# Kernel optimization log

Hardware: AMD Instinct MI355X
Metric: run time of the kernel (lower is better)

## Reference

```python
import math
import jax, jax.numpy as jnp
import numpy as np

NGRAM = 2
NUM_HEADS = 16
EMBED_DIM = 1024
HEAD_DIM = EMBED_DIM // NUM_HEADS
NUM_BUCKETS = 32
MAX_DIST = 128
REAL_T = 512
BSZ = 4
NEG = -10000.0


def _bucket_np(n):
    # unidirectional T5-style log bucket, matching _relative_positions_bucket
    n = np.maximum(n, 0)
    max_exact = NUM_BUCKETS // 2
    is_small = n < max_exact
    val = max_exact + np.log(np.maximum(n, 1) / max_exact) / math.log(MAX_DIST / max_exact) * (NUM_BUCKETS - max_exact)
    val = np.minimum(val, NUM_BUCKETS - 1).astype(np.int32)
    return np.where(is_small, n.astype(np.int32), val)


def setup_inputs() -> dict:
    key = jax.random.key(0)
    ks = jax.random.split(key, 4)
    T, B, E = REAL_T, BSZ, EMBED_DIM
    hidden_states = jax.random.normal(ks[0], ((1 + NGRAM) * T, B, E), jnp.float32)
    s = 1.0 / math.sqrt(E)  # ~xavier scale
    in_proj_weight = jax.random.uniform(ks[1], (3 * E, E), jnp.float32, -s, s)
    in_proj_bias = jnp.zeros((3 * E,), jnp.float32)
    rel_w = jax.random.uniform(ks[2], (NUM_BUCKETS * NUM_HEADS, E), jnp.float32, -s, s)
    rel_b = jnp.zeros((NUM_BUCKETS * NUM_HEADS,), jnp.float32)
    out_w = jax.random.uniform(ks[3], (E, E), jnp.float32, -s, s)
    out_b = jnp.zeros((E,), jnp.float32)
    # relative-position buckets (main stream: keys at positions 1..T)
    pos = np.arange(1, T + 1)
    i_buckets_main = np.broadcast_to(_bucket_np(pos[:, None] - pos[None, :]), (B, T, T)).copy()
    # predict stream keys: concat(main positions shifted by -1, predict positions)
    key_pos = np.concatenate([pos - 1, pos])
    i_buckets_ngram = np.broadcast_to(_bucket_np(pos[:, None] - key_pos[None, :]), (B, T, 2 * T)).copy()
    # masks
    t = np.arange(T)
    self_attn_mask = np.where(t[None, :] <= t[:, None], 0.0, NEG).astype(np.float32)  # causal [T,T]
    s_idx = np.arange(2 * T)
    allow = ((s_idx[None, :] < T) & (s_idx[None, :] <= t[:, None])) | (s_idx[None, :] == T + t[:, None])
    ngram_mask = np.broadcast_to(np.where(allow, 0.0, NEG).astype(np.float32), (NGRAM, T, 2 * T)).copy()
    return dict(
        hidden_states=hidden_states,
        in_proj_weight=in_proj_weight, in_proj_bias=in_proj_bias,
        rel_w=rel_w, rel_b=rel_b, out_w=out_w, out_b=out_b,
        self_attn_mask=jnp.asarray(self_attn_mask), ngram_mask=jnp.asarray(ngram_mask),
        i_buckets_main=jnp.asarray(i_buckets_main, jnp.int32),
        i_buckets_ngram=jnp.asarray(i_buckets_ngram, jnp.int32),
    )


def _rel_values(h, rel_w, rel_b):
    # h: [..., T, E] -> per-head bucket values [..., H, T, NUM_BUCKETS]
    vals = h @ rel_w.T + rel_b                              # [..., T, K*H]
    vals = vals.reshape(vals.shape[:-1] + (NUM_BUCKETS, NUM_HEADS))  # [..., T, K, H]
    return jnp.moveaxis(vals, (-1, -2), (-3, -1))           # [..., H, T, K]


def _forward(hidden_states, in_proj_weight, in_proj_bias, rel_w, rel_b, out_w, out_b,
             self_attn_mask, ngram_mask, i_buckets_main, i_buckets_ngram):
    tgt_len, B, E = hidden_states.shape
    T = tgt_len // (1 + NGRAM)
    H, d = NUM_HEADS, HEAD_DIM
    scaling = d ** -0.5

    qkv = hidden_states @ in_proj_weight.T + in_proj_bias
    q, k, v = jnp.split(qkv, 3, axis=-1)
    q = q * scaling

    def to_bh(x):  # [tgt_len, B, E] -> [B*H, tgt_len, d]
        return jnp.swapaxes(x.reshape(tgt_len, B * H, d), 0, 1)

    q, k, v = to_bh(q), to_bh(k), to_bh(v)
    q_main, k_main, v_main = q[:, :T], k[:, :T], v[:, :T]

    # ---- main stream ----
    aw_main = jnp.einsum('btd,bsd->bts', q_main, k_main)            # [BH,T,T]
    h_main = jnp.swapaxes(hidden_states[:T], 0, 1)                  # [B,T,E]
    vals_main = _rel_values(h_main, rel_w, rel_b)                   # [B,H,T,K]
    idx = jnp.broadcast_to(i_buckets_main[:, None], (B, H, T, T))
    rel_main = jnp.take_along_axis(vals_main, idx, axis=-1).reshape(B * H, T, T)
    aw_main = aw_main + rel_main + self_attn_mask[None]
    p_main = jax.nn.softmax(aw_main.astype(jnp.float32), axis=-1).astype(aw_main.dtype)
    attn_main = jnp.einsum('bts,bsd->btd', p_main, v_main)          # [BH,T,d]
    attn_main = jnp.swapaxes(attn_main, 0, 1).reshape(T, B, E) @ out_w.T + out_b

    # ---- ngram (predict) streams ----
    S2 = 2 * T
    q_ng = jnp.moveaxis(q[:, T:].reshape(B * H, NGRAM, T, d), 1, 0)  # [N,BH,T,d]
    k_ng = jnp.moveaxis(k[:, T:].reshape(B * H, NGRAM, T, d), 1, 0)
    v_ng = jnp.moveaxis(v[:, T:].reshape(B * H, NGRAM, T, d), 1, 0)
    k_cat = jnp.concatenate([jnp.broadcast_to(k_main[None], (NGRAM, B * H, T, d)), k_ng], axis=2)  # [N,BH,2T,d]
    v_cat = jnp.concatenate([jnp.broadcast_to(v_main[None], (NGRAM, B * H, T, d)), v_ng], axis=2)
    aw_ng = jnp.einsum('nbtd,nbsd->nbts', q_ng, k_cat)               # [N,BH,T,2T]
    h_ng = jnp.swapaxes(hidden_states[T:].reshape(NGRAM, T, B, E), 1, 2)  # [N,B,T,E]
    vals_ng = _rel_values(h_ng, rel_w, rel_b)                        # [N,B,H,T,K]
    idx2 = jnp.broadcast_to(i_buckets_ngram[None, :, None], (NGRAM, B, H, T, S2))
    rel_ng = jnp.take_along_axis(vals_ng, idx2, axis=-1).reshape(NGRAM, B * H, T, S2)
    aw_ng = aw_ng + rel_ng + ngram_mask[:, None]
    p_ng = jax.nn.softmax(aw_ng.astype(jnp.float32), axis=-1).astype(aw_ng.dtype)
    attn_ng = jnp.einsum('nbts,nbsd->nbtd', p_ng, v_cat)             # [N,BH,T,d]
    attn_ng = jnp.swapaxes(attn_ng, 1, 2).reshape(NGRAM, T, B, E) @ out_w.T + out_b

    return jnp.concatenate([attn_main, attn_ng.reshape(NGRAM * T, B, E)], axis=0)  # [(1+N)T,B,E]


def reference(hidden_states, in_proj_weight, in_proj_bias, rel_w, rel_b, out_w, out_b,
              self_attn_mask, ngram_mask, i_buckets_main, i_buckets_ngram):
    return _forward(hidden_states, in_proj_weight, in_proj_bias, rel_w, rel_b, out_w, out_b,
                    self_attn_mask, ngram_mask, i_buckets_main, i_buckets_ngram)
```

## Files before the change

kernel.cpp:

```cpp
#include <hip/hip_runtime.h>
#include <stdint.h>

#define T_LEN 512
#define NTOK  1536
#define EMB   1024
#define BS    4

typedef __bf16 bf16x8 __attribute__((ext_vector_type(8)));
typedef float  f32x4  __attribute__((ext_vector_type(4)));

__device__ __forceinline__ float bflo(unsigned short u){
  union { unsigned int i; float f; } a; a.i = ((unsigned int)u) << 16; return a.f;
}
__device__ __forceinline__ unsigned short f2bf(float f){
  union { float f; unsigned int i; } v; v.f = f;
  unsigned int x = v.i;
  return (unsigned short)((x + 0x7fffu + ((x >> 16) & 1u)) >> 16);
}

__device__ __forceinline__ void gld_lds16(const unsigned short* gptr, unsigned short* lptr){
  __builtin_amdgcn_global_load_lds(
      (const __attribute__((address_space(1))) unsigned int*)gptr,
      (__attribute__((address_space(3))) unsigned int*)lptr, 16, 0, 0);
}

__global__ __launch_bounds__(256)
void cast_k(const float* __restrict__ h, const float* __restrict__ wq,
            const float* __restrict__ rw, const float* __restrict__ ow,
            unsigned short* __restrict__ Hb, unsigned short* __restrict__ Wc,
            unsigned short* __restrict__ Ob)
{
  const size_t e = ((size_t)blockIdx.x * 256 + threadIdx.x) * 8;
  const float* src; unsigned short* dst;
  if (e < 6291456)            { src = h  + e;                 dst = Hb + e; }
  else if (e < 9437184)       { size_t o = e - 6291456;       src = wq + o; dst = Wc + o; }
  else if (e < 9961472)       { size_t o = e - 9437184;       src = rw + o; dst = Wc + 3145728 + o; }
  else                        { size_t o = e - 9961472;       src = ow + o; dst = Ob + o; }
  float4 f0 = *(const float4*)src, f1 = *(const float4*)(src + 4);
  unsigned short r[8];
  r[0]=f2bf(f0.x); r[1]=f2bf(f0.y); r[2]=f2bf(f0.z); r[3]=f2bf(f0.w);
  r[4]=f2bf(f1.x); r[5]=f2bf(f1.y); r[6]=f2bf(f1.z); r[7]=f2bf(f1.w);
  *(uint4*)dst = *(const uint4*)r;
}

template<int MODE>
__global__ __launch_bounds__(256)
void mgemm(const unsigned short* __restrict__ A,
           const unsigned short* __restrict__ W,
           const float* __restrict__ B0,
           const float* __restrict__ B1,
           unsigned short* __restrict__ Qo, unsigned short* __restrict__ Ko,
           unsigned short* __restrict__ Vo, float* __restrict__ VALS,
           float* __restrict__ OUT)
{
  constexpr int TM = (MODE == 0) ? 128 : 64;
  constexpr int NI = (MODE == 0) ? 4 : 2;
  __shared__ unsigned short As[TM*32];
  __shared__ unsigned short Bs[128*32];
  const int K = 1024;
  const int m0 = blockIdx.y * TM, n0 = blockIdx.x * 128;
  const int tid = threadIdx.x;
  const int wid = tid >> 6, lane = tid & 63;
  const int l15 = lane & 15, q8 = (lane >> 4) * 8;
  const int srow = lane >> 2, schunk = (lane & 3) * 8;
  const int wcol = (MODE == 0) ? (wid >> 1) * 64 : wid * 32;
  const int wtok = (MODE == 0) ? (wid & 1) * 64 : 0;

  f32x4 acc[NI][4];
  #pragma unroll
  for (int i=0;i<NI;i++)
    #pragma unroll
    for (int j=0;j<4;j++)
      #pragma unroll
      for (int r=0;r<4;r++) acc[i][j][r] = 0.f;

  for (int k0 = 0; k0 < K; k0 += 32) {
    if (MODE == 0) {
      #pragma unroll
      for (int p = 0; p < 2; ++p) {
        const int r0 = p*64 + wid*16;
        gld_lds16(A + (size_t)(m0 + r0 + srow)*K + k0 + schunk, &As[r0*32]);
      }
    } else {
      const int r0 = wid*16;
      gld_lds16(A + (size_t)(m0 + r0 + srow)*K + k0 + schunk, &As[r0*32]);
    }
    #pragma unroll
    for (int p = 0; p < 2; ++p) {
      const int r0 = p*64 + wid*16;
      gld_lds16(W + (size_t)(n0 + r0 + srow)*K + k0 + schunk, &Bs[r0*32]);
    }
    __syncthreads();
    bf16x8 wf[NI], hf[4];
    #pragma unroll
    for (int i=0;i<NI;i++) wf[i] = *(const bf16x8*)&Bs[(wcol + i*16 + l15)*32 + q8];
    #pragma unroll
    for (int j=0;j<4;j++)  hf[j] = *(const bf16x8*)&As[(wtok + j*16 + l15)*32 + q8];
    #pragma unroll
    for (int i=0;i<NI;i++)
      #pragma unroll
      for (int j=0;j<4;j++)
        acc[i][j] = __builtin_amdgcn_mfma_f32_16x16x32_bf16(wf[i], hf[j], acc[i][j], 0, 0, 0);
    __syncthreads();
  }

  const int rbase = (lane >> 4) * 4;
  #pragma unroll
  for (int i=0;i<NI;i++){
    const int c0 = n0 + wcol + i*16 + rbase;
    float4 b4;
    if (MODE==0) b4 = (c0 < 3072) ? *(const float4*)&B0[c0]
                                  : *(const float4*)&B1[c0-3072];
    else         b4 = *(const float4*)&B0[c0];
    #pragma unroll
    for (int j=0;j<4;j++){
      const int tokrow = m0 + wtok + j*16 + l15;
      float v[4];
      v[0]=acc[i][j][0]+b4.x; v[1]=acc[i][j][1]+b4.y;
      v[2]=acc[i][j][2]+b4.z; v[3]=acc[i][j][3]+b4.w;
      if (MODE==1){
        float4 st; st.x=v[0]; st.y=v[1]; st.z=v[2]; st.w=v[3];
        *(float4*)&OUT[(size_t)tokrow*EMB + c0] = st;
      } else {
        const int tok = tokrow >> 2, bb = tokrow & 3;
        if (c0 < 3072){
          const int which = c0 >> 10, e = c0 & 1023;
          const int h = e >> 6, d0 = e & 63;
          const float sc = (which==0) ? 0.125f : 1.0f;
          unsigned short pk[4];
          #pragma unroll
          for (int r=0;r<4;r++) pk[r] = f2bf(v[r]*sc);
          unsigned short* base = (which==0) ? Qo : (which==1) ? Ko : Vo;
          *(uint2*)&base[((size_t)(bb*16+h)*NTOK + tok)*64 + d0] = *(const uint2*)pk;
        } else {
          const int nb = (c0 - 3072) >> 4;
          #pragma unroll
          for (int r=0;r<4;r++)
            VALS[((size_t)(bb*16 + rbase + r)*NTOK + tok)*32 + nb] = v[r];
        }
      }
    }
  }
}

__global__ __launch_bounds__(256)
void vtr(const unsigned short* __restrict__ Vn, unsigned short* __restrict__ VT)
{
  __shared__ unsigned short t[64*72];
  const int bh = blockIdx.y, t0 = blockIdx.x * 64;
  const int tid = threadIdx.x;
  const int row = tid & 63, seg = tid >> 6;
  const unsigned short* src = Vn + ((size_t)bh*NTOK + t0 + row)*64 + seg*16;
  *(uint4*)&t[row*72 + seg*16]     = *(const uint4*)src;
  *(uint4*)&t[row*72 + seg*16 + 8] = *(const uint4*)(src + 8);
  __syncthreads();
  unsigned short v[16];
  #pragma unroll
  for (int k=0;k<16;k++) v[k] = t[(seg*16+k)*72 + row];
  unsigned short* dst = VT + ((size_t)bh*64 + row)*NTOK + t0 + seg*16;
  *(uint4*)dst       = *(const uint4*)&v[0];
  *(uint4*)(dst + 8) = *(const uint4*)&v[8];
}

__global__ __launch_bounds__(256, 1)
void fattn(const unsigned short* __restrict__ Q,
           const unsigned short* __restrict__ K,
           const unsigned short* __restrict__ VT,
           const float* __restrict__ VALS,
           const int* __restrict__ IBM,
           const int* __restrict__ IBN,
           unsigned short* __restrict__ OUT)
{
  __shared__ float vls[6][64*33];
  __shared__ unsigned short Pl[4][16*72];
  __shared__ int fs[513];
  __shared__ float pex[4][16];
  __shared__ float lar[4][16];

  const int pr = blockIdx.x & 3, bh = blockIdx.x >> 2;
  const int qlo = pr, qhi = 7 - pr;
  const int tid = threadIdx.x, wid = tid >> 6, lane = tid & 63;
  const int l15 = lane & 15, q4 = lane >> 4;

  fs[tid]       = IBM[(size_t)tid * T_LEN];
  fs[tid + 256] = IBM[(size_t)(tid + 256) * T_LEN];
  if (tid == 0) fs[512] = IBN[(size_t)511 * (2*T_LEN)];

  int tokbase[6];
  #pragma unroll
  for (int c=0;c<6;c++){
    const int s = c >> 1;
    const int qt = (c & 1) ? qhi : qlo;
    tokbase[c] = s*T_LEN + qt*64;
  }
  {
    const int row = tid >> 2, c8 = (tid & 3) * 8;
    #pragma unroll
    for (int c=0;c<6;c++){
      const float* vsrc = VALS + ((size_t)bh*NTOK + tokbase[c] + row)*32 + c8;
      *(float4*)&vls[c][row*33 + c8]     = *(const float4*)vsrc;
      *(float4*)&vls[c][row*33 + c8 + 4] = *(const float4*)(vsrc + 4);
    }
  }

  const unsigned short* Kbh = K  + (size_t)bh*NTOK*64;
  const unsigned short* Vbh = VT + (size_t)bh*64*NTOK;

  bf16x8 bq[6][2];
  #pragma unroll
  for (int c=0;c<6;c++){
    const unsigned short* qp = Q + ((size_t)bh*NTOK + tokbase[c] + wid*16 + l15)*64 + q4*8;
    bq[c][0] = *(const bf16x8*)qp;
    bq[c][1] = *(const bf16x8*)(qp + 32);
  }

  f32x4 o[6][4];
  float lr[6];
  #pragma unroll
  for (int c=0;c<6;c++){
    lr[c] = 0.f;
    #pragma unroll
    for (int jd=0;jd<4;jd++)
      #pragma unroll
      for (int r=0;r<4;r++) o[c][jd][r] = 0.f;
  }
  const f32x4 zero = {0.f,0.f,0.f,0.f};
  unsigned short* Pw = &Pl[wid][0];

  __syncthreads();

  for (int tile = 0; tile <= qhi; ++tile) {
    const int u0 = tile * 64;
    bf16x8 ka0[4], ka1[4], vb0[4], vb1[4];
    #pragma unroll
    for (int i=0;i<4;i++){
      const unsigned short* kp = Kbh + (size_t)(u0 + 16*i + l15)*64 + q4*8;
      ka0[i] = *(const bf16x8*)kp;  ka1[i] = *(const bf16x8*)(kp + 32);
      const unsigned short* vp = Vbh + (size_t)(16*i + l15)*NTOK + u0 + q4*8;
      vb0[i] = *(const bf16x8*)vp;  vb1[i] = *(const bf16x8*)(vp + 32);
    }
    #pragma unroll
    for (int c=0;c<6;c++){
      const int qt = (c & 1) ? qhi : qlo;
      if (tile > qt) continue;
      const int t = qt*64 + wid*16 + l15;
      const int relofs = (c >= 2) ? 1 : 0;
      f32x4 st[4];
      #pragma unroll
      for (int i=0;i<4;i++){
        st[i] = __builtin_amdgcn_mfma_f32_16x16x32_bf16(ka0[i], bq[c][0], zero, 0, 0, 0);
        st[i] = __builtin_amdgcn_mfma_f32_16x16x32_bf16(ka1[i], bq[c][1], st[i], 0, 0, 0);
      }
      float lp = 0.f;
      #pragma unroll
      for (int i=0;i<4;i++){
        unsigned short pr4[4];
        #pragma unroll
        for (int r=0;r<4;r++){
          const int u = u0 + 16*i + q4*4 + r;
          const bool ok = (u <= t);
          const int nd = ok ? (t - u + relofs) : 0;
          const float rel = vls[c][(wid*16 + l15)*33 + fs[nd]];
          float p = ok ? __expf(st[i][r] + rel) : 0.f;
          const unsigned short pb = f2bf(p);
          pr4[r] = pb;
          lp += bflo(pb);
        }
        uint2 pk;
        pk.x = (unsigned int)pr4[0] | ((unsigned int)pr4[1] << 16);
        pk.y = (unsigned int)pr4[2] | ((unsigned int)pr4[3] << 16);
        *(uint2*)&Pw[l15*72 + 16*i + q4*4] = pk;
      }
      lp += __shfl_xor(lp, 16);
      lp += __shfl_xor(lp, 32);
      lr[c] += lp;
      bf16x8 ap0 = *(const bf16x8*)&Pw[l15*72 + q4*8];
      bf16x8 ap1 = *(const bf16x8*)&Pw[l15*72 + 32 + q4*8];
      #pragma unroll
      for (int jd=0;jd<4;jd++){
        o[c][jd] = __builtin_amdgcn_mfma_f32_16x16x32_bf16(ap0, vb0[jd], o[c][jd], 0, 0, 0);
        o[c][jd] = __builtin_amdgcn_mfma_f32_16x16x32_bf16(ap1, vb1[jd], o[c][jd], 0, 0, 0);
      }
    }
  }

  #pragma unroll
  for (int c=2;c<6;c++){
    const int qtok = tokbase[c] + wid*16 + l15;
    const unsigned short* qp2 = Q + ((size_t)bh*NTOK + qtok)*64 + q4*16;
    const unsigned short* kp2 = Kbh + (size_t)qtok*64 + q4*16;
    float s = 0.f;
    #pragma unroll
    for (int cc=0;cc<2;cc++){
      bf16x8 qv = *(const bf16x8*)(qp2 + cc*8);
      bf16x8 kv = *(const bf16x8*)(kp2 + cc*8);
      #pragma unroll
      for (int e=0;e<8;e++) s += (float)qv[e] * (float)kv[e];
    }
    s += __shfl_xor(s, 16);
    s += __shfl_xor(s, 32);
    const float p = __expf(s + vls[c][(wid*16 + l15)*33 + fs[0]]);
    lr[c] += p;
    pex[wid][l15] = p;
    #pragma unroll
    for (int r=0;r<4;r++){
      const int qloc = q4*4 + r;
      const float pq = pex[wid][qloc];
      const int qtk = tokbase[c] + wid*16 + qloc;
      #pragma unroll
      for (int jd=0;jd<4;jd++){
        const float vv = bflo(Vbh[(size_t)(16*jd + l15)*NTOK + qtk]);
        o[c][jd][r] += pq * vv;
      }
    }
  }

  const int b = bh >> 4, h = bh & 15;
  #pragma unroll
  for (int c=0;c<6;c++){
    lar[wid][l15] = lr[c];
    #pragma unroll
    for (int r=0;r<4;r++){
      const int qloc = q4*4 + r;
      const float inv = 1.0f / lar[wid][qloc];
      const int qtk = tokbase[c] + wid*16 + qloc;
      unsigned short* orow = OUT + ((size_t)qtk*BS + b)*EMB + h*64 + l15;
      #pragma unroll
      for (int jd=0;jd<4;jd++)
        orow[16*jd] = f2bf(o[c][jd][r] * inv);
    }
  }
}

extern "C" void kernel_launch(void* const* d_in, const int* in_sizes, int n_in,
                              void* d_out, int out_size, void* d_ws, size_t ws_size,
                              hipStream_t stream) {
  (void)in_sizes; (void)n_in; (void)out_size; (void)ws_size;
  const float* hidden = (const float*)d_in[0];
  const float* wqkv   = (const float*)d_in[1];
  const float* bqkv   = (const float*)d_in[2];
  const float* relw   = (const float*)d_in[3];
  const float* relb   = (const float*)d_in[4];
  const float* outw   = (const float*)d_in[5];
  const float* outb   = (const float*)d_in[6];
  const int* ibm = (const int*)d_in[9];
  const int* ibn = (const int*)d_in[10];

  unsigned short* Hb  = (unsigned short*)d_ws;
  unsigned short* Wc  = Hb + (size_t)6291456;
  unsigned short* Ob  = Wc + (size_t)3670016;
  unsigned short* Qb  = Ob + (size_t)1048576;
  unsigned short* Kb  = Qb + (size_t)6291456;
  unsigned short* Vn  = Kb + (size_t)6291456;
  unsigned short* VTb = Vn + (size_t)6291456;
  float* VLS = (float*)(VTb + (size_t)6291456);
  unsigned short* ATTb = Hb;

  cast_k<<<5376, 256, 0, stream>>>(hidden, wqkv, relw, outw, Hb, Wc, Ob);
  mgemm<0><<<dim3(28, 48), 256, 0, stream>>>(Hb, Wc, bqkv, relb,
                                             Qb, Kb, Vn, VLS, nullptr);
  vtr<<<dim3(24, 64), 256, 0, stream>>>(Vn, VTb);
  fattn<<<256, 256, 0, stream>>>(Qb, Kb, VTb, VLS, ibm, ibn, ATTb);
  mgemm<1><<<dim3(8, 96), 256, 0, stream>>>(ATTb, Ob, outb, nullptr,
                                            nullptr, nullptr, nullptr, nullptr,
                                            (float*)d_out);
}
```

Measured before the change: 297.3 us.

## Fuse V transpose into QKV GEMM epilogue via LDS-staged coalesced stores

The QKV GEMM now tiles rows per batch, so each block covers 128 consecutive tokens of one batch. Its epilogue stages results in shared memory and writes Q/K rows, a transposed V and a re-laid-out relative-bucket value tensor with wide coalesced stores. This removes the separate V-transpose kernel and its extra round trip through global memory. The output GEMM also stages through LDS for coalesced float4 stores, and the attention kernel reads the new VALS layout and transposes it into LDS. The cost is extra shared memory and syncthreads in the epilogue, which may lower occupancy.

Measured after the change: 329.5 us. +10.8%, slower.

```diff
diff --git a/kernel.cpp b/kernel.cpp
--- a/kernel.cpp
+++ b/kernel.cpp
@@ -55,16 +55,21 @@
 {
   constexpr int TM = (MODE == 0) ? 128 : 64;
   constexpr int NI = (MODE == 0) ? 4 : 2;
+  constexpr int TSB = (MODE == 0) ? (128*68) : (64*132*2);
   __shared__ unsigned short As[TM*32];
   __shared__ unsigned short Bs[128*32];
+  __shared__ __align__(16) unsigned short Ts[TSB];
   const int K = 1024;
-  const int m0 = blockIdx.y * TM, n0 = blockIdx.x * 128;
+  const int n0 = blockIdx.x * 128;
   const int tid = threadIdx.x;
   const int wid = tid >> 6, lane = tid & 63;
   const int l15 = lane & 15, q8 = (lane >> 4) * 8;
   const int srow = lane >> 2, schunk = (lane & 3) * 8;
   const int wcol = (MODE == 0) ? (wid >> 1) * 64 : wid * 32;
   const int wtok = (MODE == 0) ? (wid & 1) * 64 : 0;
+  const int bb  = (MODE == 0) ? (blockIdx.y & 3) : 0;
+  const int tk0 = (MODE == 0) ? (blockIdx.y >> 2) * 128 : 0;
+  const int m0  = (MODE == 0) ? 0 : blockIdx.y * 64;
 
   f32x4 acc[NI][4];
   #pragma unroll
@@ -79,7 +84,8 @@
       #pragma unroll
       for (int p = 0; p < 2; ++p) {
         const int r0 = p*64 + wid*16;
-        gld_lds16(A + (size_t)(m0 + r0 + srow)*K + k0 + schunk, &As[r0*32]);
+        const size_t arow = (size_t)((tk0 + r0 + srow)*4 + bb);
+        gld_lds16(A + arow*K + k0 + schunk, &As[r0*32]);
       }
     } else {
       const int r0 = wid*16;
@@ -103,63 +109,114 @@
         acc[i][j] = __builtin_amdgcn_mfma_f32_16x16x32_bf16(wf[i], hf[j], acc[i][j], 0, 0, 0);
     __syncthreads();
   }
-
   const int rbase = (lane >> 4) * 4;
-  #pragma unroll
-  for (int i=0;i<NI;i++){
-    const int c0 = n0 + wcol + i*16 + rbase;
-    float4 b4;
-    if (MODE==0) b4 = (c0 < 3072) ? *(const float4*)&B0[c0]
-                                  : *(const float4*)&B1[c0-3072];
-    else         b4 = *(const float4*)&B0[c0];
-    #pragma unroll
-    for (int j=0;j<4;j++){
-      const int tokrow = m0 + wtok + j*16 + l15;
-      float v[4];
-      v[0]=acc[i][j][0]+b4.x; v[1]=acc[i][j][1]+b4.y;
-      v[2]=acc[i][j][2]+b4.z; v[3]=acc[i][j][3]+b4.w;
-      if (MODE==1){
-        float4 st; st.x=v[0]; st.y=v[1]; st.z=v[2]; st.w=v[3];
-        *(float4*)&OUT[(size_t)tokrow*EMB + c0] = st;
-      } else {
-        const int tok = tokrow >> 2, bb = tokrow & 3;
-        if (c0 < 3072){
-          const int which = c0 >> 10, e = c0 & 1023;
-          const int h = e >> 6, d0 = e & 63;
-          const float sc = (which==0) ? 0.125f : 1.0f;
-          unsigned short pk[4];
+
+  if (MODE == 1) {
+    float* Tsf = (float*)Ts;
+    #pragma unroll
+    for (int i=0;i<NI;i++){
+      const int c0l = wcol + i*16 + rbase;
+      float4 b4 = *(const float4*)&B0[n0 + c0l];
+      #pragma unroll
+      for (int j=0;j<4;j++){
+        float4 st; st.x=acc[i][j][0]+b4.x; st.y=acc[i][j][1]+b4.y;
+        st.z=acc[i][j][2]+b4.z; st.w=acc[i][j][3]+b4.w;
+        *(float4*)&Tsf[(j*16 + l15)*132 + c0l] = st;
+      }
+    }
+    __syncthreads();
+    const int tokl = tid >> 2, seg = (tid & 3) * 32;
+    float* orow = OUT + (size_t)(m0 + tokl)*EMB + n0 + seg;
+    #pragma unroll
+    for (int q=0;q<8;q++)
+      *(float4*)(orow + q*4) = *(const float4*)&Tsf[tokl*132 + seg + q*4];
+    return;
+  }
+
+  #pragma unroll
+  for (int ch = 0; ch < 2; ++ch) {
+    const int col64 = n0 + ch*64;
+    const bool isrel = (col64 >= 3072);
+    const int which = col64 >> 10;
+    const int hh = (col64 & 1023) >> 6;
+
+    if (!isrel && which <= 1) {
+      if ((wid >> 1) == ch) {
+        const float sc = (which==0) ? 0.125f : 1.0f;
+        #pragma unroll
+        for (int i=0;i<4;i++){
+          const int cg = col64 + i*16 + rbase;
+          float4 b4 = *(const float4*)&B0[cg];
           #pragma unroll
-          for (int r=0;r<4;r++) pk[r] = f2bf(v[r]*sc);
-          unsigned short* base = (which==0) ? Qo : (which==1) ? Ko : Vo;
-          *(uint2*)&base[((size_t)(bb*16+h)*NTOK + tok)*64 + d0] = *(const uint2*)pk;
-        } else {
-          const int nb = (c0 - 3072) >> 4;
+          for (int j=0;j<4;j++){
+            unsigned short pk[4];
+            pk[0]=f2bf((acc[i][j][0]+b4.x)*sc); pk[1]=f2bf((acc[i][j][1]+b4.y)*sc);
+            pk[2]=f2bf((acc[i][j][2]+b4.z)*sc); pk[3]=f2bf((acc[i][j][3]+b4.w)*sc);
+            *(uint2*)&Ts[(wtok + j*16 + l15)*68 + i*16 + rbase] = *(const uint2*)pk;
+          }
+        }
+      }
+      __syncthreads();
+      const int tokl = tid >> 1, chk = (tid & 1) * 32;
+      unsigned short* base = (which==0) ? Qo : Ko;
+      unsigned short* dst = base + ((size_t)(bb*16+hh)*NTOK + tk0 + tokl)*64 + chk;
+      #pragma unroll
+      for (int q=0;q<4;q++)
+        *(uint4*)(dst + q*8) = *(const uint4*)&Ts[tokl*68 + chk + q*8];
+      __syncthreads();
+    } else if (!isrel) {
+      if ((wid >> 1) == ch) {
+        #pragma unroll
+        for (int i=0;i<4;i++){
+          const int cg = col64 + i*16 + rbase;
+          float4 b4 = *(const float4*)&B0[cg];
           #pragma unroll
-          for (int r=0;r<4;r++)
-            VALS[((size_t)(bb*16 + rbase + r)*NTOK + tok)*32 + nb] = v[r];
+          for (int j=0;j<4;j++){
+            #pragma unroll
+            for (int r=0;r<4;r++)
+              Ts[(i*16 + rbase + r)*132 + wtok + j*16 + l15]
+                = f2bf(acc[i][j][r] + ((const float*)&b4)[r]);
+          }
         }
       }
-    }
-  }
-}
-
-__global__ __launch_bounds__(256)
-void vtr(const unsigned short* __restrict__ Vn, unsigned short* __restrict__ VT)
-{
-  __shared__ unsigned short t[64*72];
-  const int bh = blockIdx.y, t0 = blockIdx.x * 64;
-  const int tid = threadIdx.x;
-  const int row = tid & 63, seg = tid >> 6;
-  const unsigned short* src = Vn + ((size_t)bh*NTOK + t0 + row)*64 + seg*16;
-  *(uint4*)&t[row*72 + seg*16]     = *(const uint4*)src;
-  *(uint4*)&t[row*72 + seg*16 + 8] = *(const uint4*)(src + 8);
-  __syncthreads();
-  unsigned short v[16];
-  #pragma unroll
-  for (int k=0;k<16;k++) v[k] = t[(seg*16+k)*72 + row];
-  unsigned short* dst = VT + ((size_t)bh*64 + row)*NTOK + t0 + seg*16;
-  *(uint4*)dst       = *(const uint4*)&v[0];
-  *(uint4*)(dst + 8) = *(const uint4*)&v[8];
+      __syncthreads();
+      const int cl = tid >> 2, chk = (tid & 3) * 32;
+      unsigned short* dst = Vo + ((size_t)(bb*16+hh)*64 + cl)*NTOK + tk0 + chk;
+      #pragma unroll
+      for (int q=0;q<4;q++)
+        *(uint4*)(dst + q*8) = *(const uint4*)&Ts[cl*132 + chk + q*8];
+      __syncthreads();
+    } else {
+      float* Tsf = (float*)Ts;
+      #pragma unroll
+      for (int p = 0; p < 2; ++p) {
+        if ((wid >> 1) == ch) {
+          #pragma unroll
+          for (int ii=0; ii<2; ++ii){
+            const int i = p*2 + ii;
+            const int cg = col64 + i*16 + rbase;
+            float4 b4 = *(const float4*)&B1[cg - 3072];
+            #pragma unroll
+            for (int j=0;j<4;j++){
+              #pragma unroll
+              for (int r=0;r<4;r++)
+                Tsf[(ii*16 + rbase + r)*132 + wtok + j*16 + l15]
+                  = acc[i][j][r] + ((const float*)&b4)[r];
+            }
+          }
+        }
+        __syncthreads();
+        const int cl = tid >> 3, chk = (tid & 7) * 16;
+        const int e2 = (col64 - 3072) + p*32 + cl;
+        const int nb = e2 >> 4, hr = e2 & 15;
+        float* dst = VALS + ((size_t)(bb*32+nb)*16 + hr)*NTOK + tk0 + chk;
+        #pragma unroll
+        for (int q=0;q<4;q++)
+          *(float4*)(dst + q*4) = *(const float4*)&Tsf[cl*132 + chk + q*4];
+        __syncthreads();
+      }
+    }
+  }
 }
 
 __global__ __launch_bounds__(256, 1)
@@ -194,12 +251,16 @@
     tokbase[c] = s*T_LEN + qt*64;
   }
   {
-    const int row = tid >> 2, c8 = (tid & 3) * 8;
+    const int nb = tid >> 3, t8 = (tid & 7) * 8;
+    const float* vr = VALS + ((size_t)((bh >> 4)*32 + nb)*16 + (bh & 15))*NTOK;
     #pragma unroll
     for (int c=0;c<6;c++){
-      const float* vsrc = VALS + ((size_t)bh*NTOK + tokbase[c] + row)*32 + c8;
-      *(float4*)&vls[c][row*33 + c8]     = *(const float4*)vsrc;
-      *(float4*)&vls[c][row*33 + c8 + 4] = *(const float4*)(vsrc + 4);
+      float4 a = *(const float4*)(vr + tokbase[c] + t8);
+      float4 b = *(const float4*)(vr + tokbase[c] + t8 + 4);
+      vls[c][(t8+0)*33 + nb] = a.x; vls[c][(t8+1)*33 + nb] = a.y;
+      vls[c][(t8+2)*33 + nb] = a.z; vls[c][(t8+3)*33 + nb] = a.w;
+      vls[c][(t8+4)*33 + nb] = b.x; vls[c][(t8+5)*33 + nb] = b.y;
+      vls[c][(t8+6)*33 + nb] = b.z; vls[c][(t8+7)*33 + nb] = b.w;
     }
   }
 
@@ -351,15 +412,13 @@
   unsigned short* Ob  = Wc + (size_t)3670016;
   unsigned short* Qb  = Ob + (size_t)1048576;
   unsigned short* Kb  = Qb + (size_t)6291456;
-  unsigned short* Vn  = Kb + (size_t)6291456;
-  unsigned short* VTb = Vn + (size_t)6291456;
+  unsigned short* VTb = Kb + (size_t)6291456;
   float* VLS = (float*)(VTb + (size_t)6291456);
   unsigned short* ATTb = Hb;
 
   cast_k<<<5376, 256, 0, stream>>>(hidden, wqkv, relw, outw, Hb, Wc, Ob);
   mgemm<0><<<dim3(28, 48), 256, 0, stream>>>(Hb, Wc, bqkv, relb,
-                                             Qb, Kb, Vn, VLS, nullptr);
-  vtr<<<dim3(24, 64), 256, 0, stream>>>(Vn, VTb);
+                                             Qb, Kb, VTb, VLS, nullptr);
   fattn<<<256, 256, 0, stream>>>(Qb, Kb, VTb, VLS, ibm, ibn, ATTb);
   mgemm<1><<<dim3(8, 96), 256, 0, stream>>>(ATTb, Ob, outb, nullptr,
                                             nullptr, nullptr, nullptr, nullptr,
```
